# Kernel tuning notes

Measured on AMD Instinct MI355X. Metric: run time of the kernel, lower is better.

The kernel has to match this reference:

```python
import jax, jax.numpy as jnp
import numpy as np

B, LQ, LK, E, HID, H = 4, 1024, 2048, 512, 512, 8


def _ln(x, g, b, eps=1e-5):
    mu = jnp.mean(x, -1, keepdims=True)
    var = jnp.mean((x - mu) ** 2, -1, keepdims=True)
    return (x - mu) * jax.lax.rsqrt(var + eps) * g + b


def _mha(q_in, k_in, v_in, Wq, bq, Wk, bk, Wv, bv, Wo, bo, nheads, q_valid, k_valid):
    # torch nn.MultiheadAttention (batch_first, eval/dropout=0) math
    Bq, Lq, Em = q_in.shape
    Lk = k_in.shape[1]
    hd = Em // nheads
    q = (q_in @ Wq.T + bq).reshape(Bq, Lq, nheads, hd)
    k = (k_in @ Wk.T + bk).reshape(Bq, Lk, nheads, hd)
    v = (v_in @ Wv.T + bv).reshape(Bq, Lk, nheads, hd)
    scale = 1.0 / np.sqrt(hd).astype(np.float32)
    s = jnp.einsum('bqhd,bkhd->bhqk', q, k) * scale
    if k_valid is not None:
        # valid query rows may only attend to valid key columns
        s = jnp.where(k_valid[:, None, None, :], s, jnp.finfo(s.dtype).min)
    w = jax.nn.softmax(s, axis=-1)
    # rows beyond a sample's length are fully masked in the torch nested path
    # (softmax -> NaN, later nan_to_num'd to 0); we zero them directly.
    w = jnp.where(q_valid[:, None, :, None], w, 0.0)
    o = jnp.einsum('bhqk,bkhd->bqhd', w, v).reshape(Bq, Lq, Em)
    return o @ Wo.T + bo, jnp.mean(w, axis=1)  # weights averaged over heads


def setup_inputs() -> dict:
    key = jax.random.key(0)
    ks = jax.random.split(key, 32)
    p = lambda i, shape: 0.02 * jax.random.normal(ks[i], shape, dtype=jnp.float32)
    inp = {
        'queries': jax.random.normal(ks[0], (B, LQ, E), dtype=jnp.float32),
        'keys': jax.random.normal(ks[1], (B, LK, E), dtype=jnp.float32),
        'q_len': jax.random.randint(ks[2], (B,), 1, LQ + 1),
        # cross-attention params
        'cWq': p(3, (E, E)), 'cbq': jnp.zeros((E,)),
        'cWk': p(4, (E, E)), 'cbk': jnp.zeros((E,)),
        'cWv': p(5, (E, E)), 'cbv': jnp.zeros((E,)),
        'cWo': p(6, (E, E)), 'cbo': jnp.zeros((E,)),
        # self-attention params
        'sWq': p(7, (HID, HID)), 'sbq': jnp.zeros((HID,)),
        'sWk': p(8, (HID, HID)), 'sbk': jnp.zeros((HID,)),
        'sWv': p(9, (HID, HID)), 'sbv': jnp.zeros((HID,)),
        'sWo': p(10, (HID, HID)), 'sbo': jnp.zeros((HID,)),
        # ffn + norms
        'Wf': p(11, (HID, E)), 'bf': jnp.zeros((HID,)),
        'g_cross': jnp.ones((E,)), 'b_cross': jnp.zeros((E,)),
        'g_ffn': jnp.ones((HID,)), 'b_ffn': jnp.zeros((HID,)),
        'g_self': jnp.ones((HID,)), 'b_self': jnp.zeros((HID,)),
    }
    return inp


def reference(queries, keys, q_len,
              cWq, cbq, cWk, cbk, cWv, cbv, cWo, cbo,
              sWq, sbq, sWk, sbk, sWv, sbv, sWo, sbo,
              Wf, bf, g_cross, b_cross, g_ffn, b_ffn, g_self, b_self):
    valid = jnp.arange(LQ)[None, :] < q_len[:, None]  # [B, LQ] ragged lengths
    q = jnp.where(valid[..., None], queries, 0.0)     # nested -> padded with 0
    # cross attention: valid rows attend to ALL keys (per the nested mask)
    cross, weights = _mha(q, keys, keys, cWq, cbq, cWk, cbk, cWv, cbv, cWo, cbo,
                          H, valid, None)
    q = _ln(jax.nn.silu(cross + q), g_cross, b_cross)
    f = q @ Wf.T + bf
    q = _ln(jax.nn.silu(q + f), g_ffn, b_ffn)  # q_dim == hidden_dim branch
    q = jnp.where(valid[..., None], q, 0.0)    # torch.nan_to_num on padded rows
    # self attention: valid rows attend only to valid rows of the same sample
    so, _ = _mha(q, q, q, sWq, sbq, sWk, sbk, sWv, sbv, sWo, sbo, H, valid, valid)
    q = _ln(jax.nn.silu(q + so), g_self, b_self)
    q = jnp.where(valid[..., None], q, 0.0)    # padded rows discarded by unbind
    return q, weights
```

## Files before the change

kernel.cpp:

```cpp
#include <hip/hip_runtime.h>

#define BB 4
#define SLQ 1024
#define SLK 2048
#define EE 512
#define HH 8
#define HD 64

typedef unsigned short u16;
typedef __attribute__((ext_vector_type(8))) short s16x8;
typedef __attribute__((ext_vector_type(4))) float f32x4;

__device__ __forceinline__ float bf2f(u16 u) {
  union { unsigned int i; float f; } v; v.i = ((unsigned int)u) << 16; return v.f;
}
__device__ __forceinline__ u16 f2bf(float f) {
  union { float f; unsigned int i; } v; v.f = f;
  unsigned int i = v.i;
  return (u16)((i + 0x7fffu + ((i >> 16) & 1u)) >> 16);
}

__device__ __forceinline__ void async16(const u16* g, u16* l) {
  __builtin_amdgcn_global_load_lds(
      (const __attribute__((address_space(1))) unsigned int*)g,
      (__attribute__((address_space(3))) unsigned int*)l, 16, 0, 0);
}

template<int BM, int BN, int MODE, int SKIPQ>
__global__ __launch_bounds__(256, 2)
void gemm_nt(const u16* __restrict__ A, const u16* __restrict__ Bm,
             const float* __restrict__ bias, u16* __restrict__ C,
             int M, int N, int K, int lda, int ldb, int ldc,
             long sAz, long sBz, long sCz, float alpha, int Lsub,
             const int* __restrict__ qlen)
{
  constexpr int WTM = BM / 2, WTN = BN / 2;
  constexpr int MI = WTM / 16, NI = WTN / 16;

  const int z = blockIdx.z;
  const int tileM = blockIdx.y * BM;
  const int tileN = blockIdx.x * BN;

  if (SKIPQ == 1) { if (tileM >= qlen[z >> 3]) return; }
  if (SKIPQ == 2) { int b = tileM >> 10; if ((tileM & 1023) >= qlen[b]) return; }

  __shared__ __align__(16) u16 smem[(BM + BN) * 32];
  u16* ldsA = smem;
  u16* ldsB = smem + BM * 32;

  const int t = threadIdx.x;
  const int lane = t & 63;
  const int wave = t >> 6;
  const int waveM = wave >> 1;
  const int waveN = wave & 1;
  const int lm = lane & 15;
  const int kg = lane >> 4;

  const u16* Ab = A + (long)z * sAz + (long)tileM * lda;
  const u16* Bb = Bm + (long)z * sBz + (long)tileN * ldb;

  f32x4 acc[MI][NI];
#pragma unroll
  for (int i = 0; i < MI; ++i)
#pragma unroll
    for (int j = 0; j < NI; ++j) acc[i][j] = (f32x4){0.f, 0.f, 0.f, 0.f};

  for (int kt = 0; kt < K; kt += 32) {
    __syncthreads();
#pragma unroll
    for (int i = 0; i < (BM * 4) / 256; ++i) {
      int c = i * 256 + t;
      async16(Ab + (long)(c >> 2) * lda + kt + (c & 3) * 8, ldsA + (c - lane) * 8);
    }
#pragma unroll
    for (int i = 0; i < (BN * 4) / 256; ++i) {
      int c = i * 256 + t;
      async16(Bb + (long)(c >> 2) * ldb + kt + (c & 3) * 8, ldsB + (c - lane) * 8);
    }
    __syncthreads();

    s16x8 aF[MI], bF[NI];
#pragma unroll
    for (int i = 0; i < MI; ++i)
      aF[i] = *(const s16x8*)&ldsA[(waveM * WTM + i * 16 + lm) * 32 + kg * 8];
#pragma unroll
    for (int j = 0; j < NI; ++j)
      bF[j] = *(const s16x8*)&ldsB[(waveN * WTN + j * 16 + lm) * 32 + kg * 8];
#pragma unroll
    for (int i = 0; i < MI; ++i)
#pragma unroll
      for (int j = 0; j < NI; ++j)
        acc[i][j] = __builtin_amdgcn_mfma_f32_16x16x32_bf16(aF[i], bF[j], acc[i][j], 0, 0, 0);
  }

  if (MODE == 0) {
#pragma unroll
    for (int c = 0; c < BM / 32; ++c) {
      const int rlo = c * 32;
      __syncthreads();
#pragma unroll
      for (int i = 0; i < MI; ++i) {
        int mbase = waveM * WTM + i * 16;
        if (mbase >= rlo && mbase < rlo + 32) {
#pragma unroll
          for (int j = 0; j < NI; ++j) {
            int n = waveN * WTN + j * 16 + lm;
            float bv = bias ? bias[tileN + n] : 0.0f;
#pragma unroll
            for (int r = 0; r < 4; ++r) {
              int m = mbase + kg * 4 + r;
              smem[(m - rlo) * BN + n] = f2bf(acc[i][j][r] * alpha + bv);
            }
          }
        }
      }
      __syncthreads();
#pragma unroll
      for (int v = 0; v < (32 * BN) / (256 * 8); ++v) {
        int idx = v * 256 + t;
        int row = idx / (BN / 8), col8 = idx % (BN / 8);
        *(uint4*)&C[(long)z * sCz + (long)(tileM + rlo + row) * ldc + tileN + col8 * 8] =
            *(const uint4*)&smem[row * BN + col8 * 8];
      }
    }
  } else if (MODE == 2) {
    constexpr int PAD = BM + 8;
    const int bb = tileM / Lsub;
    const int l0 = tileM - bb * Lsub;
#pragma unroll
    for (int c = 0; c < BN / 32; ++c) {
      __syncthreads();
#pragma unroll
      for (int j = 0; j < NI; ++j) {
        int nloc = waveN * WTN + j * 16 + lm;
        if (nloc >= c * 32 && nloc < c * 32 + 32) {
          int nl = nloc - c * 32;
          float bv = bias ? bias[tileN + nloc] : 0.0f;
#pragma unroll
          for (int i = 0; i < MI; ++i)
#pragma unroll
            for (int r = 0; r < 4; ++r) {
              int mm = waveM * WTM + i * 16 + kg * 4 + r;
              smem[nl * PAD + mm] = f2bf(acc[i][j][r] * alpha + bv);
            }
        }
      }
      __syncthreads();
#pragma unroll
      for (int v = 0; v < (32 * BM) / (256 * 8); ++v) {
        int idx = v * 256 + t;
        int nl = idx / (BM / 8), m8 = idx % (BM / 8);
        int n = tileN + c * 32 + nl;
        int h = n >> 6, d = n & 63;
        *(uint4*)&C[((long)(bb * HH + h) * HD + d) * Lsub + l0 + m8 * 8] =
            *(const uint4*)&smem[nl * PAD + m8 * 8];
      }
    }
  } else {
#pragma unroll
    for (int j = 0; j < NI; ++j) {
      int n = tileN + waveN * WTN + j * 16 + lm;
      float bv = bias ? bias[n] : 0.0f;
#pragma unroll
      for (int i = 0; i < MI; ++i) {
#pragma unroll
        for (int r = 0; r < 4; ++r) {
          int m = tileM + waveM * WTM + i * 16 + kg * 4 + r;
          float v = acc[i][j][r] * alpha + bv;
          int b = m / Lsub, l = m - b * Lsub;
          int h = n >> 6, d = n & 63;
          C[(((long)(b * HH + h) * Lsub + l) << 6) + d] = f2bf(v);
        }
      }
    }
  }
}

__global__ __launch_bounds__(256)
void softmax_stats_wmean(const u16* __restrict__ S, float* __restrict__ outw,
                         float2* __restrict__ stats, const int* __restrict__ qlen) {
  int row = blockIdx.x;
  int b = row >> 10, q = row & 1023;
  int t = threadIdx.x, lane = t & 63, w = t >> 6;
  float* wr = outw + (long)row * SLK;
  if (q >= qlen[b]) {
    float4 z = {0.f, 0.f, 0.f, 0.f};
    *(float4*)(wr + t * 8) = z; *(float4*)(wr + t * 8 + 4) = z;
    return;
  }
  __shared__ float acc4[4][2048];
#pragma unroll
  for (int hh = 0; hh < 2; ++hh) {
    int h = 2 * w + hh;
    const u16* p = S + ((long)((b * HH + h) * SLQ + q)) * SLK;
    float x[4][8];
    float m = -1e30f;
#pragma unroll
    for (int c = 0; c < 4; ++c) {
      s16x8 v = *(const s16x8*)(p + c * 512 + lane * 8);
#pragma unroll
      for (int j = 0; j < 8; ++j) { x[c][j] = bf2f((u16)v[j]); m = fmaxf(m, x[c][j]); }
    }
#pragma unroll
    for (int o = 1; o <= 32; o <<= 1) m = fmaxf(m, __shfl_xor(m, o));
    float s = 0.f;
#pragma unroll
    for (int c = 0; c < 4; ++c)
#pragma unroll
      for (int j = 0; j < 8; ++j) { x[c][j] = __expf(x[c][j] - m); s += x[c][j]; }
#pragma unroll
    for (int o = 1; o <= 32; o <<= 1) s += __shfl_xor(s, o);
    if (lane == 0) stats[(long)(b * HH + h) * SLQ + q] = (float2){m, s};
    float sc = 0.125f / s;
#pragma unroll
    for (int c = 0; c < 4; ++c) {
      float4 v0 = {x[c][0] * sc, x[c][1] * sc, x[c][2] * sc, x[c][3] * sc};
      float4 v1 = {x[c][4] * sc, x[c][5] * sc, x[c][6] * sc, x[c][7] * sc};
      if (hh == 0) {
        *(float4*)&acc4[w][c * 512 + lane * 8] = v0;
        *(float4*)&acc4[w][c * 512 + lane * 8 + 4] = v1;
      } else {
        float4 a0 = *(const float4*)&acc4[w][c * 512 + lane * 8];
        float4 a1 = *(const float4*)&acc4[w][c * 512 + lane * 8 + 4];
        a0.x += v0.x; a0.y += v0.y; a0.z += v0.z; a0.w += v0.w;
        a1.x += v1.x; a1.y += v1.y; a1.z += v1.z; a1.w += v1.w;
        *(float4*)&acc4[w][c * 512 + lane * 8] = a0;
        *(float4*)&acc4[w][c * 512 + lane * 8 + 4] = a1;
      }
    }
  }
  __syncthreads();
#pragma unroll
  for (int u = 0; u < 2; ++u) {
    int k = t * 8 + u * 4;
    float4 s0 = *(const float4*)&acc4[0][k];
    float4 s1 = *(const float4*)&acc4[1][k];
    float4 s2 = *(const float4*)&acc4[2][k];
    float4 s3 = *(const float4*)&acc4[3][k];
    float4 o = {s0.x + s1.x + s2.x + s3.x, s0.y + s1.y + s2.y + s3.y,
                s0.z + s1.z + s2.z + s3.z, s0.w + s1.w + s2.w + s3.w};
    *(float4*)(wr + k) = o;
  }
}

__global__ __launch_bounds__(256, 2)
void pv_cross(const u16* __restrict__ S, const u16* __restrict__ Vt,
              const float2* __restrict__ stats, float* __restrict__ Opart,
              const int* __restrict__ qlen)
{
  const int qt = blockIdx.x;
  const int bh = blockIdx.y;
  const int kc = blockIdx.z;
  const int b = bh >> 3;
  if (qt * 64 >= qlen[b]) return;

  __shared__ __align__(16) u16 Vl[64 * 136];

  const int t = threadIdx.x, lane = t & 63, w = t >> 6;
  const int lm = lane & 15, quad = lane >> 4;

  const int qrow = qt * 64 + w * 16 + lm;
  const u16* Sb = S + ((long)bh * SLQ + qrow) * SLK;
  const u16* Vb = Vt + (long)bh * HD * SLK;
  const float mrow = stats[(long)bh * SLQ + qrow].x;

  f32x4 O[4];
#pragma unroll
  for (int n = 0; n < 4; ++n) O[n] = (f32x4){0.f, 0.f, 0.f, 0.f};

  for (int ks = 0; ks < 4; ++ks) {
    const int k0 = kc * 512 + ks * 128;
    __syncthreads();
    for (int c = t; c < 1024; c += 256) {
      int d = c >> 4, c16 = c & 15;
      *(uint4*)&Vl[d * 136 + c16 * 8] = *(const uint4*)(Vb + (long)d * SLK + k0 + c16 * 8);
    }
    __syncthreads();
#pragma unroll
    for (int kk = 0; kk < 4; ++kk) {
      s16x8 raw = *(const s16x8*)(Sb + k0 + kk * 32 + quad * 8);
      s16x8 aP;
#pragma unroll
      for (int j = 0; j < 8; ++j)
        aP[j] = (short)f2bf(__expf(bf2f((u16)raw[j]) - mrow));
#pragma unroll
      for (int n = 0; n < 4; ++n) {
        s16x8 bV = *(const s16x8*)&Vl[(n * 16 + lm) * 136 + kk * 32 + quad * 8];
        O[n] = __builtin_amdgcn_mfma_f32_16x16x32_bf16(aP, bV, O[n], 0, 0, 0);
      }
    }
  }

#pragma unroll
  for (int r = 0; r < 4; ++r) {
    int qr2 = qt * 64 + w * 16 + quad * 4 + r;
#pragma unroll
    for (int n = 0; n < 4; ++n)
      Opart[(((long)bh * SLQ + qr2) * 4 + kc) * 64 + n * 16 + lm] = O[n][r];
  }
}

__global__ __launch_bounds__(256)
void pv_combine_cross(const float* __restrict__ Opart, const float2* __restrict__ stats,
                      u16* __restrict__ attn, const int* __restrict__ qlen)
{
  int gr = blockIdx.x * 16 + (threadIdx.x >> 4);
  int bh = gr >> 10, q = gr & 1023;
  int b = bh >> 3, h = bh & 7;
  if (q >= qlen[b]) return;
  int d = (threadIdx.x & 15) * 4;
  float ax = 0.f, ay = 0.f, az = 0.f, aw = 0.f;
#pragma unroll
  for (int c = 0; c < 4; ++c) {
    float4 o = *(const float4*)&Opart[((long)gr * 4 + c) * 64 + d];
    ax += o.x; ay += o.y; az += o.z; aw += o.w;
  }
  float inv = 1.0f / stats[gr].y;
  unsigned int lo = (unsigned int)f2bf(ax * inv) | ((unsigned int)f2bf(ay * inv) << 16);
  unsigned int hi = (unsigned int)f2bf(az * inv) | ((unsigned int)f2bf(aw * inv) << 16);
  *(uint2*)&attn[((long)b * SLQ + q) * EE + h * HD + d] = (uint2){lo, hi};
}

__global__ __launch_bounds__(256, 3)
void self_flash_chunk(const u16* __restrict__ Qc, const u16* __restrict__ Kc,
                      const u16* __restrict__ Vt, float* __restrict__ Opart,
                      float* __restrict__ ml, const int* __restrict__ qlen)
{
  const int qt = blockIdx.x;
  const int bh = blockIdx.y;
  const int ck = blockIdx.z;
  const int b = bh >> 3;
  const int kmax = qlen[b];
  const int k0 = ck * 128;
  if (qt * 64 >= kmax || k0 >= kmax) return;

  __shared__ __align__(16) u16 Kt[128 * 72];
  __shared__ __align__(16) u16 Vl[64 * 136];
  __shared__ __align__(16) u16 Pl[4 * 16 * 136];

  const int t = threadIdx.x, lane = t & 63, w = t >> 6;
  const int col = lane & 15, quad = lane >> 4;

  const u16* Qb = Qc + (long)bh * SLQ * HD;
  const u16* Kb = Kc + (long)bh * SLQ * HD;
  const u16* Vb = Vt + (long)bh * HD * SLQ;

  for (int c = t; c < 1024; c += 256) {
    int r = c >> 3, c8 = c & 7;
    *(uint4*)&Kt[r * 72 + c8 * 8] = *(const uint4*)(Kb + (long)(k0 + r) * HD + c8 * 8);
  }
  for (int c = t; c < 1024; c += 256) {
    int d = c >> 4, c16 = c & 15;
    *(uint4*)&Vl[d * 136 + c16 * 8] = *(const uint4*)(Vb + (long)d * SLQ + k0 + c16 * 8);
  }
  s16x8 aQ[2];
#pragma unroll
  for (int kk = 0; kk < 2; ++kk)
    aQ[kk] = *(const s16x8*)(Qb + (long)(qt * 64 + w * 16 + col) * HD + kk * 32 + quad * 8);
  __syncthreads();

  f32x4 s[8];
#pragma unroll
  for (int j = 0; j < 8; ++j) s[j] = (f32x4){0.f, 0.f, 0.f, 0.f};
#pragma unroll
  for (int j = 0; j < 8; ++j)
#pragma unroll
    for (int kk = 0; kk < 2; ++kk) {
      s16x8 bK = *(const s16x8*)&Kt[(j * 16 + col) * 72 + kk * 32 + quad * 8];
      s[j] = __builtin_amdgcn_mfma_f32_16x16x32_bf16(aQ[kk], bK, s[j], 0, 0, 0);
    }
#pragma unroll
  for (int j = 0; j < 8; ++j) {
    bool ok = (k0 + j * 16 + col) < kmax;
#pragma unroll
    for (int r = 0; r < 4; ++r)
      s[j][r] = ok ? s[j][r] * 0.125f : -1e30f;
  }
  float mr[4], lr[4];
#pragma unroll
  for (int r = 0; r < 4; ++r) {
    float tm = s[0][r];
#pragma unroll
    for (int j = 1; j < 8; ++j) tm = fmaxf(tm, s[j][r]);
#pragma unroll
    for (int o = 1; o <= 8; o <<= 1) tm = fmaxf(tm, __shfl_xor(tm, o));
    mr[r] = tm;
    float ps = 0.f;
#pragma unroll
    for (int j = 0; j < 8; ++j) {
      float p = __expf(s[j][r] - tm);
      s[j][r] = p;
      ps += p;
    }
#pragma unroll
    for (int o = 1; o <= 8; o <<= 1) ps += __shfl_xor(ps, o);
    lr[r] = ps;
  }
  u16* Pw = Pl + w * 16 * 136;
#pragma unroll
  for (int j = 0; j < 8; ++j)
#pragma unroll
    for (int r = 0; r < 4; ++r)
      Pw[(quad * 4 + r) * 136 + j * 16 + col] = f2bf(s[j][r]);

  f32x4 O[4];
#pragma unroll
  for (int n = 0; n < 4; ++n) O[n] = (f32x4){0.f, 0.f, 0.f, 0.f};
#pragma unroll
  for (int kk = 0; kk < 4; ++kk) {
    s16x8 aP = *(const s16x8*)&Pw[col * 136 + kk * 32 + quad * 8];
#pragma unroll
    for (int n = 0; n < 4; ++n) {
      s16x8 bV = *(const s16x8*)&Vl[(n * 16 + col) * 136 + kk * 32 + quad * 8];
      O[n] = __builtin_amdgcn_mfma_f32_16x16x32_bf16(aP, bV, O[n], 0, 0, 0);
    }
  }
#pragma unroll
  for (int r = 0; r < 4; ++r) {
    int q = qt * 64 + w * 16 + quad * 4 + r;
    long gq = (long)bh * SLQ + q;
#pragma unroll
    for (int n = 0; n < 4; ++n)
      Opart[(gq * 8 + ck) * 64 + n * 16 + col] = O[n][r];
    if (col == 0) {
      ml[(gq * 8 + ck) * 2] = mr[r];
      ml[(gq * 8 + ck) * 2 + 1] = lr[r];
    }
  }
}

__global__ __launch_bounds__(256)
void self_combine(const float* __restrict__ Opart, const float* __restrict__ ml,
                  u16* __restrict__ attn, const int* __restrict__ qlen)
{
  int gr = blockIdx.x * 16 + (threadIdx.x >> 4);
  int bh = gr >> 10, q = gr & 1023;
  int b = bh >> 3, h = bh & 7;
  int kmax = qlen[b];
  if (q >= kmax) return;
  int NC = (kmax + 127) >> 7;
  int d = (threadIdx.x & 15) * 4;
  long base = (long)gr * 8;
  float M = -1e30f;
  for (int c = 0; c < NC; ++c) M = fmaxf(M, ml[(base + c) * 2]);
  float L = 0.f;
  float ax = 0.f, ay = 0.f, az = 0.f, aw = 0.f;
  for (int c = 0; c < NC; ++c) {
    float wgt = __expf(ml[(base + c) * 2] - M);
    L += ml[(base + c) * 2 + 1] * wgt;
    float4 o = *(const float4*)&Opart[(base + c) * 64 + d];
    ax += o.x * wgt; ay += o.y * wgt; az += o.z * wgt; aw += o.w * wgt;
  }
  float inv = 1.0f / L;
  unsigned int lo = (unsigned int)f2bf(ax * inv) | ((unsigned int)f2bf(ay * inv) << 16);
  unsigned int hi = (unsigned int)f2bf(az * inv) | ((unsigned int)f2bf(aw * inv) << 16);
  *(uint2*)&attn[((long)b * SLQ + q) * EE + h * HD + d] = (uint2){lo, hi};
}

__global__ __launch_bounds__(256)
void cvt_all(const float* __restrict__ queries, const float* __restrict__ keys,
             const int* __restrict__ qlen,
             const float* w0, const float* w1, const float* w2, const float* w3,
             const float* w4, const float* w5, const float* w6, const float* w7,
             const float* w8,
             u16* __restrict__ q0, u16* __restrict__ keysb, u16* __restrict__ Wb) {
  int blk = blockIdx.x;
  int t = threadIdx.x;
  const float* src;
  u16* dst;
  long off;
  bool mask = false;
  int b = 0, q = 0;
  if (blk < 1024) {
    off = (long)blk * 2048 + t * 8;
    int row = (int)(off >> 9);
    b = row >> 10; q = row & 1023;
    mask = true;
    src = queries; dst = q0;
  } else if (blk < 3072) {
    off = (long)(blk - 1024) * 2048 + t * 8;
    src = keys; dst = keysb;
  } else {
    int mat = (blk - 3072) >> 7, part = (blk - 3072) & 127;
    const float* srcs[9] = {w0, w1, w2, w3, w4, w5, w6, w7, w8};
    src = srcs[mat];
    off = (long)part * 2048 + t * 8;
    dst = Wb + (long)mat * EE * EE;
  }
  s16x8 o = (s16x8){0, 0, 0, 0, 0, 0, 0, 0};
  if (!mask || q < qlen[b]) {
    float4 a = *(const float4*)&src[off];
    float4 c = *(const float4*)&src[off + 4];
    o[0] = (short)f2bf(a.x); o[1] = (short)f2bf(a.y);
    o[2] = (short)f2bf(a.z); o[3] = (short)f2bf(a.w);
    o[4] = (short)f2bf(c.x); o[5] = (short)f2bf(c.y);
    o[6] = (short)f2bf(c.z); o[7] = (short)f2bf(c.w);
  }
  *(s16x8*)&dst[off] = o;
}

__device__ __forceinline__ float blockSum(float v, float* red4) {
#pragma unroll
  for (int o = 32; o; o >>= 1) v += __shfl_xor(v, o);
  if ((threadIdx.x & 63) == 0) red4[threadIdx.x >> 6] = v;
  __syncthreads();
  v = red4[0] + red4[1] + red4[2] + red4[3];
  __syncthreads();
  return v;
}

template<int OUTF32>
__global__ __launch_bounds__(256)
void silu_ln_kernel(const u16* __restrict__ x1, const u16* __restrict__ x2,
                    const float* __restrict__ g, const float* __restrict__ beta,
                    const int* __restrict__ qlen, void* __restrict__ outv, int mode) {
  int row = blockIdx.x;
  int b = row >> 10, q = row & 1023;
  int t = threadIdx.x;
  if (mode && q >= qlen[b]) {
    if (mode == 1) {
      if (OUTF32) {
        float* o = (float*)outv + (long)row * EE;
        o[2 * t] = 0.f; o[2 * t + 1] = 0.f;
      } else {
        u16* o = (u16*)outv + (long)row * EE;
        *(unsigned int*)&o[2 * t] = 0u;
      }
    }
    return;
  }
  __shared__ float red4[4];
  const u16* p1 = x1 + (long)row * EE;
  const u16* p2 = x2 + (long)row * EE;
  float a0 = bf2f(p1[2 * t]) + bf2f(p2[2 * t]);
  float a1 = bf2f(p1[2 * t + 1]) + bf2f(p2[2 * t + 1]);
  a0 = a0 / (1.f + __expf(-a0));
  a1 = a1 / (1.f + __expf(-a1));
  float mu = blockSum(a0 + a1, red4) * (1.f / 512.f);
  float d0 = a0 - mu, d1 = a1 - mu;
  float var = blockSum(d0 * d0 + d1 * d1, red4) * (1.f / 512.f);
  float rs = rsqrtf(var + 1e-5f);
  float r0 = d0 * rs * g[2 * t] + beta[2 * t];
  float r1 = d1 * rs * g[2 * t + 1] + beta[2 * t + 1];
  if (OUTF32) {
    float* o = (float*)outv + (long)row * EE;
    o[2 * t] = r0; o[2 * t + 1] = r1;
  } else {
    u16* o = (u16*)outv + (long)row * EE;
    o[2 * t] = f2bf(r0); o[2 * t + 1] = f2bf(r1);
  }
}

extern "C" void kernel_launch(void* const* d_in, const int* in_sizes, int n_in,
                              void* d_out, int out_size, void* d_ws, size_t ws_size,
                              hipStream_t stream) {
  const float* queries = (const float*)d_in[0];
  const float* keys    = (const float*)d_in[1];
  const int*   qlen    = (const int*)d_in[2];
  const float* cWq = (const float*)d_in[3],  *cbq = (const float*)d_in[4];
  const float* cWk = (const float*)d_in[5],  *cbk = (const float*)d_in[6];
  const float* cWv = (const float*)d_in[7],  *cbv = (const float*)d_in[8];
  const float* cWo = (const float*)d_in[9],  *cbo = (const float*)d_in[10];
  const float* sWq = (const float*)d_in[11], *sbq = (const float*)d_in[12];
  const float* sWk = (const float*)d_in[13], *sbk = (const float*)d_in[14];
  const float* sWv = (const float*)d_in[15], *sbv = (const float*)d_in[16];
  const float* sWo = (const float*)d_in[17], *sbo = (const float*)d_in[18];
  const float* Wf  = (const float*)d_in[19], *bfb = (const float*)d_in[20];
  const float* g_cross = (const float*)d_in[21], *b_cross = (const float*)d_in[22];
  const float* g_ffn   = (const float*)d_in[23], *b_ffn   = (const float*)d_in[24];
  const float* g_self  = (const float*)d_in[25], *b_self  = (const float*)d_in[26];

  float* out_q = (float*)d_out;
  float* out_w = out_q + (long)BB * SLQ * EE;

  u16* ws = (u16*)d_ws;
  u16* S     = ws;
  u16* Qc    = S   + (long)BB * HH * SLQ * SLK;
  u16* Kc    = Qc  + (long)BB * HH * SLQ * HD;
  u16* Vt    = Kc  + (long)BB * HH * SLK * HD;
  u16* q0    = Vt  + (long)BB * HH * SLK * HD;
  u16* keysb = q0  + (long)BB * SLQ * EE;
  u16* attn  = keysb + (long)BB * SLK * EE;
  u16* proj  = attn + (long)BB * SLQ * EE;
  u16* q1    = proj + (long)BB * SLQ * EE;
  u16* fbuf  = q1  + (long)BB * SLQ * EE;
  u16* q2    = fbuf + (long)BB * SLQ * EE;
  u16* Wb    = q2  + (long)BB * SLQ * EE;
  const long WSLOT = (long)EE * EE;
  float*  CpF  = (float*)(Wb + 9 * WSLOT);
  float2* stat = (float2*)(CpF + 8388608);

  float* OpS = (float*)S;
  float* mlS = (float*)(S + 33554432);

  u16* bWq = Wb + 0 * WSLOT; u16* bWk = Wb + 1 * WSLOT; u16* bWv = Wb + 2 * WSLOT;
  u16* bWo = Wb + 3 * WSLOT; u16* bsWq = Wb + 4 * WSLOT; u16* bsWk = Wb + 5 * WSLOT;
  u16* bsWv = Wb + 6 * WSLOT; u16* bsWo = Wb + 7 * WSLOT; u16* bWf = Wb + 8 * WSLOT;

  dim3 blk(256);
  const int MQ = BB * SLQ;
  const int MK = BB * SLK;

  cvt_all<<<dim3(3072 + 9 * 128), blk, 0, stream>>>(
      queries, keys, qlen, cWq, cWk, cWv, cWo, sWq, sWk, sWv, sWo, Wf, q0, keysb, Wb);

  gemm_nt<64, 64, 1, 2><<<dim3(EE / 64, MQ / 64, 1), blk, 0, stream>>>(
      q0, bWq, cbq, Qc, MQ, EE, EE, EE, EE, 0, 0, 0, 0, 1.0f, SLQ, qlen);
  gemm_nt<64, 64, 1, 0><<<dim3(EE / 64, MK / 64, 1), blk, 0, stream>>>(
      keysb, bWk, cbk, Kc, MK, EE, EE, EE, EE, 0, 0, 0, 0, 1.0f, SLK, qlen);
  gemm_nt<64, 64, 2, 0><<<dim3(EE / 64, MK / 64, 1), blk, 0, stream>>>(
      keysb, bWv, cbv, Vt, MK, EE, EE, EE, EE, 0, 0, 0, 0, 1.0f, SLK, qlen);

  gemm_nt<128, 128, 0, 1><<<dim3(SLK / 128, SLQ / 128, BB * HH), blk, 0, stream>>>(
      Qc, Kc, nullptr, S, SLQ, SLK, HD, HD, HD, SLK,
      (long)SLQ * HD, (long)SLK * HD, (long)SLQ * SLK, 0.125f, 0, qlen);

  softmax_stats_wmean<<<dim3(BB * SLQ), blk, 0, stream>>>(S, out_w, stat, qlen);

  pv_cross<<<dim3(16, 32, 4), blk, 0, stream>>>(S, Vt, stat, CpF, qlen);
  pv_combine_cross<<<dim3(2048), blk, 0, stream>>>(CpF, stat, attn, qlen);

  gemm_nt<64, 64, 0, 2><<<dim3(EE / 64, MQ / 64, 1), blk, 0, stream>>>(
      attn, bWo, cbo, proj, MQ, EE, EE, EE, EE, EE, 0, 0, 0, 1.0f, SLQ, qlen);

  silu_ln_kernel<0><<<dim3(MQ), blk, 0, stream>>>(proj, q0, g_cross, b_cross, qlen, q1, 2);

  gemm_nt<64, 64, 0, 2><<<dim3(EE / 64, MQ / 64, 1), blk, 0, stream>>>(
      q1, bWf, bfb, fbuf, MQ, EE, EE, EE, EE, EE, 0, 0, 0, 1.0f, SLQ, qlen);

  silu_ln_kernel<0><<<dim3(MQ), blk, 0, stream>>>(q1, fbuf, g_ffn, b_ffn, qlen, q2, 1);

  gemm_nt<64, 64, 1, 2><<<dim3(EE / 64, MQ / 64, 1), blk, 0, stream>>>(
      q2, bsWq, sbq, Qc, MQ, EE, EE, EE, EE, 0, 0, 0, 0, 1.0f, SLQ, qlen);
  gemm_nt<64, 64, 1, 2><<<dim3(EE / 64, MQ / 64, 1), blk, 0, stream>>>(
      q2, bsWk, sbk, Kc, MQ, EE, EE, EE, EE, 0, 0, 0, 0, 1.0f, SLQ, qlen);
  gemm_nt<64, 64, 2, 2><<<dim3(EE / 64, MQ / 64, 1), blk, 0, stream>>>(
      q2, bsWv, sbv, Vt, MQ, EE, EE, EE, EE, 0, 0, 0, 0, 1.0f, SLQ, qlen);

  self_flash_chunk<<<dim3(16, 32, 8), blk, 0, stream>>>(Qc, Kc, Vt, OpS, mlS, qlen);
  self_combine<<<dim3(2048), blk, 0, stream>>>(OpS, mlS, attn, qlen);

  gemm_nt<64, 64, 0, 2><<<dim3(EE / 64, MQ / 64, 1), blk, 0, stream>>>(
      attn, bsWo, sbo, proj, MQ, EE, EE, EE, EE, EE, 0, 0, 0, 1.0f, SLQ, qlen);

  silu_ln_kernel<1><<<dim3(MQ), blk, 0, stream>>>(q2, proj, g_self, b_self, qlen, out_q, 1);
}
```

Before: 349.5 us.

## Batch QKV projections, bf16 partials, per-wave epilogue, longer self-attn chunks

```diff
diff --git a/kernel.cpp b/kernel.cpp
--- a/kernel.cpp
+++ b/kernel.cpp
@@ -36,6 +36,10 @@
 {
   constexpr int WTM = BM / 2, WTN = BN / 2;
   constexpr int MI = WTM / 16, NI = WTN / 16;
+  constexpr int EPAD = WTN + 8;
+  constexpr int SM1 = (BM + BN) * 32;
+  constexpr int SM2 = (MODE == 0) ? 4 * WTM * EPAD : 0;
+  constexpr int SM = (SM1 > SM2) ? SM1 : SM2;
 
   const int z = blockIdx.z;
   const int tileM = blockIdx.y * BM;
@@ -44,7 +48,7 @@
   if (SKIPQ == 1) { if (tileM >= qlen[z >> 3]) return; }
   if (SKIPQ == 2) { int b = tileM >> 10; if ((tileM & 1023) >= qlen[b]) return; }
 
-  __shared__ __align__(16) u16 smem[(BM + BN) * 32];
+  __shared__ __align__(16) u16 smem[SM];
   u16* ldsA = smem;
   u16* ldsB = smem + BM * 32;
 
@@ -94,36 +98,132 @@
   }
 
   if (MODE == 0) {
-#pragma unroll
-    for (int c = 0; c < BM / 32; ++c) {
-      const int rlo = c * 32;
-      __syncthreads();
+    u16* ep = smem + wave * (WTM * EPAD);
+    __syncthreads();
+#pragma unroll
+    for (int i = 0; i < MI; ++i)
+#pragma unroll
+      for (int j = 0; j < NI; ++j) {
+        int n = waveN * WTN + j * 16 + lm;
+        float bv = bias ? bias[tileN + n] : 0.0f;
+#pragma unroll
+        for (int r = 0; r < 4; ++r)
+          ep[(i * 16 + kg * 4 + r) * EPAD + j * 16 + lm] = f2bf(acc[i][j][r] * alpha + bv);
+      }
+    const long Crow = (long)z * sCz + (long)(tileM + waveM * WTM) * ldc + tileN + waveN * WTN;
+#pragma unroll
+    for (int it = 0; it < (WTM * WTN) / 512; ++it) {
+      int idx = it * 64 + lane;
+      int row = idx / (WTN / 8), seg = idx % (WTN / 8);
+      *(uint4*)&C[Crow + (long)row * ldc + seg * 8] =
+          *(const uint4*)&ep[row * EPAD + seg * 8];
+    }
+  } else {
+#pragma unroll
+    for (int j = 0; j < NI; ++j) {
+      int n = tileN + waveN * WTN + j * 16 + lm;
+      float bv = bias ? bias[n] : 0.0f;
 #pragma unroll
       for (int i = 0; i < MI; ++i) {
-        int mbase = waveM * WTM + i * 16;
-        if (mbase >= rlo && mbase < rlo + 32) {
-#pragma unroll
-          for (int j = 0; j < NI; ++j) {
-            int n = waveN * WTN + j * 16 + lm;
-            float bv = bias ? bias[tileN + n] : 0.0f;
-#pragma unroll
-            for (int r = 0; r < 4; ++r) {
-              int m = mbase + kg * 4 + r;
-              smem[(m - rlo) * BN + n] = f2bf(acc[i][j][r] * alpha + bv);
-            }
-          }
+#pragma unroll
+        for (int r = 0; r < 4; ++r) {
+          int m = tileM + waveM * WTM + i * 16 + kg * 4 + r;
+          float v = acc[i][j][r] * alpha + bv;
+          int b = m / Lsub, l = m - b * Lsub;
+          int h = n >> 6, d = n & 63;
+          C[(((long)(b * HH + h) * Lsub + l) << 6) + d] = f2bf(v);
         }
       }
-      __syncthreads();
-#pragma unroll
-      for (int v = 0; v < (32 * BN) / (256 * 8); ++v) {
-        int idx = v * 256 + t;
-        int row = idx / (BN / 8), col8 = idx % (BN / 8);
-        *(uint4*)&C[(long)z * sCz + (long)(tileM + rlo + row) * ldc + tileN + col8 * 8] =
-            *(const uint4*)&smem[row * BN + col8 * 8];
-      }
-    }
-  } else if (MODE == 2) {
+    }
+  }
+}
+
+template<int BM, int BN, int SKIPQ, int NPROJ>
+__global__ __launch_bounds__(256, 2)
+void gemm_proj(const u16* __restrict__ A,
+               const u16* B0, const u16* B1, const u16* B2,
+               const float* bias0, const float* bias1, const float* bias2,
+               u16* C0, u16* C1, u16* C2,
+               int M, int lda, int Lsub, const int* __restrict__ qlen)
+{
+  constexpr int WTM = BM / 2, WTN = BN / 2;
+  constexpr int MI = WTM / 16, NI = WTN / 16;
+
+  const int z = blockIdx.z;
+  const int tileM = blockIdx.y * BM;
+  const int tileN = blockIdx.x * BN;
+  if (SKIPQ == 2) { int b = tileM >> 10; if ((tileM & 1023) >= qlen[b]) return; }
+
+  const u16* Bm = (z == 0) ? B0 : (z == 1) ? B1 : B2;
+  const float* bias = (z == 0) ? bias0 : (z == 1) ? bias1 : bias2;
+  u16* C = (z == 0) ? C0 : (z == 1) ? C1 : C2;
+  const bool tr = (z == NPROJ - 1);
+
+  __shared__ __align__(16) u16 smem[(BM + BN) * 32];
+  u16* ldsA = smem;
+  u16* ldsB = smem + BM * 32;
+
+  const int t = threadIdx.x;
+  const int lane = t & 63;
+  const int wave = t >> 6;
+  const int waveM = wave >> 1;
+  const int waveN = wave & 1;
+  const int lm = lane & 15;
+  const int kg = lane >> 4;
+
+  const u16* Ab = A + (long)tileM * lda;
+  const u16* Bb = Bm + (long)tileN * EE;
+
+  f32x4 acc[MI][NI];
+#pragma unroll
+  for (int i = 0; i < MI; ++i)
+#pragma unroll
+    for (int j = 0; j < NI; ++j) acc[i][j] = (f32x4){0.f, 0.f, 0.f, 0.f};
+
+  for (int kt = 0; kt < EE; kt += 32) {
+    __syncthreads();
+#pragma unroll
+    for (int i = 0; i < (BM * 4) / 256; ++i) {
+      int c = i * 256 + t;
+      async16(Ab + (long)(c >> 2) * lda + kt + (c & 3) * 8, ldsA + (c - lane) * 8);
+    }
+#pragma unroll
+    for (int i = 0; i < (BN * 4) / 256; ++i) {
+      int c = i * 256 + t;
+      async16(Bb + (long)(c >> 2) * EE + kt + (c & 3) * 8, ldsB + (c - lane) * 8);
+    }
+    __syncthreads();
+
+    s16x8 aF[MI], bF[NI];
+#pragma unroll
+    for (int i = 0; i < MI; ++i)
+      aF[i] = *(const s16x8*)&ldsA[(waveM * WTM + i * 16 + lm) * 32 + kg * 8];
+#pragma unroll
+    for (int j = 0; j < NI; ++j)
+      bF[j] = *(const s16x8*)&ldsB[(waveN * WTN + j * 16 + lm) * 32 + kg * 8];
+#pragma unroll
+    for (int i = 0; i < MI; ++i)
+#pragma unroll
+      for (int j = 0; j < NI; ++j)
+        acc[i][j] = __builtin_amdgcn_mfma_f32_16x16x32_bf16(aF[i], bF[j], acc[i][j], 0, 0, 0);
+  }
+
+  if (!tr) {
+#pragma unroll
+    for (int j = 0; j < NI; ++j) {
+      int n = tileN + waveN * WTN + j * 16 + lm;
+      float bv = bias[n];
+#pragma unroll
+      for (int i = 0; i < MI; ++i)
+#pragma unroll
+        for (int r = 0; r < 4; ++r) {
+          int m = tileM + waveM * WTM + i * 16 + kg * 4 + r;
+          int b = m / Lsub, l = m - b * Lsub;
+          int h = n >> 6, d = n & 63;
+          C[(((long)(b * HH + h) * Lsub + l) << 6) + d] = f2bf(acc[i][j][r] + bv);
+        }
+    }
+  } else {
     constexpr int PAD = BM + 8;
     const int bb = tileM / Lsub;
     const int l0 = tileM - bb * Lsub;
@@ -135,13 +235,13 @@
         int nloc = waveN * WTN + j * 16 + lm;
         if (nloc >= c * 32 && nloc < c * 32 + 32) {
           int nl = nloc - c * 32;
-          float bv = bias ? bias[tileN + nloc] : 0.0f;
+          float bv = bias[tileN + nloc];
 #pragma unroll
           for (int i = 0; i < MI; ++i)
 #pragma unroll
             for (int r = 0; r < 4; ++r) {
               int mm = waveM * WTM + i * 16 + kg * 4 + r;
-              smem[nl * PAD + mm] = f2bf(acc[i][j][r] * alpha + bv);
+              smem[nl * PAD + mm] = f2bf(acc[i][j][r] + bv);
             }
         }
       }
@@ -154,23 +254,6 @@
         int h = n >> 6, d = n & 63;
         *(uint4*)&C[((long)(bb * HH + h) * HD + d) * Lsub + l0 + m8 * 8] =
             *(const uint4*)&smem[nl * PAD + m8 * 8];
-      }
-    }
-  } else {
-#pragma unroll
-    for (int j = 0; j < NI; ++j) {
-      int n = tileN + waveN * WTN + j * 16 + lm;
-      float bv = bias ? bias[n] : 0.0f;
-#pragma unroll
-      for (int i = 0; i < MI; ++i) {
-#pragma unroll
-        for (int r = 0; r < 4; ++r) {
-          int m = tileM + waveM * WTM + i * 16 + kg * 4 + r;
-          float v = acc[i][j][r] * alpha + bv;
-          int b = m / Lsub, l = m - b * Lsub;
-          int h = n >> 6, d = n & 63;
-          C[(((long)(b * HH + h) * Lsub + l) << 6) + d] = f2bf(v);
-        }
       }
     }
   }
@@ -245,7 +328,7 @@
 
 __global__ __launch_bounds__(256, 2)
 void pv_cross(const u16* __restrict__ S, const u16* __restrict__ Vt,
-              const float2* __restrict__ stats, float* __restrict__ Opart,
+              const float2* __restrict__ stats, u16* __restrict__ Opart,
               const int* __restrict__ qlen)
 {
   const int qt = blockIdx.x;
@@ -296,12 +379,12 @@
     int qr2 = qt * 64 + w * 16 + quad * 4 + r;
 #pragma unroll
     for (int n = 0; n < 4; ++n)
-      Opart[(((long)bh * SLQ + qr2) * 4 + kc) * 64 + n * 16 + lm] = O[n][r];
+      Opart[(((long)bh * SLQ + qr2) * 4 + kc) * 64 + n * 16 + lm] = f2bf(O[n][r]);
   }
 }
 
 __global__ __launch_bounds__(256)
-void pv_combine_cross(const float* __restrict__ Opart, const float2* __restrict__ stats,
+void pv_combine_cross(const u16* __restrict__ Opart, const float2* __restrict__ stats,
                       u16* __restrict__ attn, const int* __restrict__ qlen)
 {
   int gr = blockIdx.x * 16 + (threadIdx.x >> 4);
@@ -312,8 +395,8 @@
   float ax = 0.f, ay = 0.f, az = 0.f, aw = 0.f;
 #pragma unroll
   for (int c = 0; c < 4; ++c) {
-    float4 o = *(const float4*)&Opart[((long)gr * 4 + c) * 64 + d];
-    ax += o.x; ay += o.y; az += o.z; aw += o.w;
+    const u16* p = Opart + ((long)gr * 4 + c) * 64 + d;
+    ax += bf2f(p[0]); ay += bf2f(p[1]); az += bf2f(p[2]); aw += bf2f(p[3]);
   }
   float inv = 1.0f / stats[gr].y;
   unsigned int lo = (unsigned int)f2bf(ax * inv) | ((unsigned int)f2bf(ay * inv) << 16);
@@ -323,16 +406,15 @@
 
 __global__ __launch_bounds__(256, 3)
 void self_flash_chunk(const u16* __restrict__ Qc, const u16* __restrict__ Kc,
-                      const u16* __restrict__ Vt, float* __restrict__ Opart,
-                      float* __restrict__ ml, const int* __restrict__ qlen)
+                      const u16* __restrict__ Vt, u16* __restrict__ Opart,
+                      float2* __restrict__ ml, const int* __restrict__ qlen)
 {
   const int qt = blockIdx.x;
   const int bh = blockIdx.y;
   const int ck = blockIdx.z;
   const int b = bh >> 3;
   const int kmax = qlen[b];
-  const int k0 = ck * 128;
-  if (qt * 64 >= kmax || k0 >= kmax) return;
+  if (qt * 64 >= kmax || ck * 256 >= kmax) return;
 
   __shared__ __align__(16) u16 Kt[128 * 72];
   __shared__ __align__(16) u16 Vl[64 * 136];
@@ -345,92 +427,103 @@
   const u16* Kb = Kc + (long)bh * SLQ * HD;
   const u16* Vb = Vt + (long)bh * HD * SLQ;
 
-  for (int c = t; c < 1024; c += 256) {
-    int r = c >> 3, c8 = c & 7;
-    *(uint4*)&Kt[r * 72 + c8 * 8] = *(const uint4*)(Kb + (long)(k0 + r) * HD + c8 * 8);
-  }
-  for (int c = t; c < 1024; c += 256) {
-    int d = c >> 4, c16 = c & 15;
-    *(uint4*)&Vl[d * 136 + c16 * 8] = *(const uint4*)(Vb + (long)d * SLQ + k0 + c16 * 8);
-  }
   s16x8 aQ[2];
 #pragma unroll
   for (int kk = 0; kk < 2; ++kk)
     aQ[kk] = *(const s16x8*)(Qb + (long)(qt * 64 + w * 16 + col) * HD + kk * 32 + quad * 8);
-  __syncthreads();
-
-  f32x4 s[8];
-#pragma unroll
-  for (int j = 0; j < 8; ++j) s[j] = (f32x4){0.f, 0.f, 0.f, 0.f};
-#pragma unroll
-  for (int j = 0; j < 8; ++j)
-#pragma unroll
-    for (int kk = 0; kk < 2; ++kk) {
-      s16x8 bK = *(const s16x8*)&Kt[(j * 16 + col) * 72 + kk * 32 + quad * 8];
-      s[j] = __builtin_amdgcn_mfma_f32_16x16x32_bf16(aQ[kk], bK, s[j], 0, 0, 0);
-    }
-#pragma unroll
-  for (int j = 0; j < 8; ++j) {
-    bool ok = (k0 + j * 16 + col) < kmax;
-#pragma unroll
-    for (int r = 0; r < 4; ++r)
-      s[j][r] = ok ? s[j][r] * 0.125f : -1e30f;
-  }
+
+  f32x4 O[4];
   float mr[4], lr[4];
 #pragma unroll
-  for (int r = 0; r < 4; ++r) {
-    float tm = s[0][r];
-#pragma unroll
-    for (int j = 1; j < 8; ++j) tm = fmaxf(tm, s[j][r]);
-#pragma unroll
-    for (int o = 1; o <= 8; o <<= 1) tm = fmaxf(tm, __shfl_xor(tm, o));
-    mr[r] = tm;
-    float ps = 0.f;
+  for (int n = 0; n < 4; ++n) O[n] = (f32x4){0.f, 0.f, 0.f, 0.f};
+#pragma unroll
+  for (int r = 0; r < 4; ++r) { mr[r] = -1e30f; lr[r] = 0.f; }
+
+  u16* Pw = Pl + w * 16 * 136;
+
+  for (int kt = 0; kt < 2; ++kt) {
+    const int k0 = ck * 256 + kt * 128;
+    if (k0 >= kmax) break;
+    __syncthreads();
+    for (int c = t; c < 1024; c += 256) {
+      int r = c >> 3, c8 = c & 7;
+      *(uint4*)&Kt[r * 72 + c8 * 8] = *(const uint4*)(Kb + (long)(k0 + r) * HD + c8 * 8);
+    }
+    for (int c = t; c < 1024; c += 256) {
+      int d = c >> 4, c16 = c & 15;
+      *(uint4*)&Vl[d * 136 + c16 * 8] = *(const uint4*)(Vb + (long)d * SLQ + k0 + c16 * 8);
+    }
+    __syncthreads();
+
+    f32x4 s[8];
+#pragma unroll
+    for (int j = 0; j < 8; ++j) s[j] = (f32x4){0.f, 0.f, 0.f, 0.f};
+#pragma unroll
+    for (int j = 0; j < 8; ++j)
+#pragma unroll
+      for (int kk = 0; kk < 2; ++kk) {
+        s16x8 bK = *(const s16x8*)&Kt[(j * 16 + col) * 72 + kk * 32 + quad * 8];
+        s[j] = __builtin_amdgcn_mfma_f32_16x16x32_bf16(aQ[kk], bK, s[j], 0, 0, 0);
+      }
 #pragma unroll
     for (int j = 0; j < 8; ++j) {
-      float p = __expf(s[j][r] - tm);
-      s[j][r] = p;
-      ps += p;
-    }
-#pragma unroll
-    for (int o = 1; o <= 8; o <<= 1) ps += __shfl_xor(ps, o);
-    lr[r] = ps;
-  }
-  u16* Pw = Pl + w * 16 * 136;
-#pragma unroll
-  for (int j = 0; j < 8; ++j)
-#pragma unroll
-    for (int r = 0; r < 4; ++r)
-      Pw[(quad * 4 + r) * 136 + j * 16 + col] = f2bf(s[j][r]);
-
-  f32x4 O[4];
-#pragma unroll
-  for (int n = 0; n < 4; ++n) O[n] = (f32x4){0.f, 0.f, 0.f, 0.f};
-#pragma unroll
-  for (int kk = 0; kk < 4; ++kk) {
-    s16x8 aP = *(const s16x8*)&Pw[col * 136 + kk * 32 + quad * 8];
-#pragma unroll
-    for (int n = 0; n < 4; ++n) {
-      s16x8 bV = *(const s16x8*)&Vl[(n * 16 + col) * 136 + kk * 32 + quad * 8];
-      O[n] = __builtin_amdgcn_mfma_f32_16x16x32_bf16(aP, bV, O[n], 0, 0, 0);
-    }
-  }
+      bool ok = (k0 + j * 16 + col) < kmax;
+#pragma unroll
+      for (int r = 0; r < 4; ++r)
+        s[j][r] = ok ? s[j][r] * 0.125f : -1e30f;
+    }
+#pragma unroll
+    for (int r = 0; r < 4; ++r) {
+      float tm = s[0][r];
+#pragma unroll
+      for (int j = 1; j < 8; ++j) tm = fmaxf(tm, s[j][r]);
+#pragma unroll
+      for (int o = 1; o <= 8; o <<= 1) tm = fmaxf(tm, __shfl_xor(tm, o));
+      float mnew = fmaxf(mr[r], tm);
+      float alpha = __expf(mr[r] - mnew);
+      mr[r] = mnew;
+      float ps = 0.f;
+#pragma unroll
+      for (int j = 0; j < 8; ++j) {
+        float p = __expf(s[j][r] - mnew);
+        s[j][r] = p;
+        ps += p;
+      }
+#pragma unroll
+      for (int o = 1; o <= 8; o <<= 1) ps += __shfl_xor(ps, o);
+      lr[r] = lr[r] * alpha + ps;
+#pragma unroll
+      for (int n = 0; n < 4; ++n) O[n][r] *= alpha;
+    }
+#pragma unroll
+    for (int j = 0; j < 8; ++j)
+#pragma unroll
+      for (int r = 0; r < 4; ++r)
+        Pw[(quad * 4 + r) * 136 + j * 16 + col] = f2bf(s[j][r]);
+#pragma unroll
+    for (int kk = 0; kk < 4; ++kk) {
+      s16x8 aP = *(const s16x8*)&Pw[col * 136 + kk * 32 + quad * 8];
+#pragma unroll
+      for (int n = 0; n < 4; ++n) {
+        s16x8 bV = *(const s16x8*)&Vl[(n * 16 + col) * 136 + kk * 32 + quad * 8];
+        O[n] = __builtin_amdgcn_mfma_f32_16x16x32_bf16(aP, bV, O[n], 0, 0, 0);
+      }
+    }
+  }
+
 #pragma unroll
   for (int r = 0; r < 4; ++r) {
     int q = qt * 64 + w * 16 + quad * 4 + r;
     long gq = (long)bh * SLQ + q;
 #pragma unroll
     for (int n = 0; n < 4; ++n)
-      Opart[(gq * 8 + ck) * 64 + n * 16 + col] = O[n][r];
-    if (col == 0) {
-      ml[(gq * 8 + ck) * 2] = mr[r];
-      ml[(gq * 8 + ck) * 2 + 1] = lr[r];
-    }
+      Opart[(gq * 4 + ck) * 64 + n * 16 + col] = f2bf(O[n][r]);
+    if (col == 0) ml[gq * 4 + ck] = (float2){mr[r], lr[r]};
   }
 }
 
 __global__ __launch_bounds__(256)
-void self_combine(const float* __restrict__ Opart, const float* __restrict__ ml,
+void self_combine(const u16* __restrict__ Opart, const float2* __restrict__ ml,
                   u16* __restrict__ attn, const int* __restrict__ qlen)
 {
   int gr = blockIdx.x * 16 + (threadIdx.x >> 4);
@@ -438,18 +531,20 @@
   int b = bh >> 3, h = bh & 7;
   int kmax = qlen[b];
   if (q >= kmax) return;
-  int NC = (kmax + 127) >> 7;
+  int NC = (kmax + 255) >> 8;
   int d = (threadIdx.x & 15) * 4;
-  long base = (long)gr * 8;
+  long base = (long)gr * 4;
   float M = -1e30f;
-  for (int c = 0; c < NC; ++c) M = fmaxf(M, ml[(base + c) * 2]);
+  for (int c = 0; c < NC; ++c) M = fmaxf(M, ml[base + c].x);
   float L = 0.f;
   float ax = 0.f, ay = 0.f, az = 0.f, aw = 0.f;
   for (int c = 0; c < NC; ++c) {
-    float wgt = __expf(ml[(base + c) * 2] - M);
-    L += ml[(base + c) * 2 + 1] * wgt;
-    float4 o = *(const float4*)&Opart[(base + c) * 64 + d];
-    ax += o.x * wgt; ay += o.y * wgt; az += o.z * wgt; aw += o.w * wgt;
+    float2 st = ml[base + c];
+    float wgt = __expf(st.x - M);
+    L += st.y * wgt;
+    const u16* p = Opart + (base + c) * 64 + d;
+    ax += bf2f(p[0]) * wgt; ay += bf2f(p[1]) * wgt;
+    az += bf2f(p[2]) * wgt; aw += bf2f(p[3]) * wgt;
   }
   float inv = 1.0f / L;
   unsigned int lo = (unsigned int)f2bf(ax * inv) | ((unsigned int)f2bf(ay * inv) << 16);
@@ -587,11 +682,11 @@
   u16* q2    = fbuf + (long)BB * SLQ * EE;
   u16* Wb    = q2  + (long)BB * SLQ * EE;
   const long WSLOT = (long)EE * EE;
-  float*  CpF  = (float*)(Wb + 9 * WSLOT);
-  float2* stat = (float2*)(CpF + 8388608);
-
-  float* OpS = (float*)S;
-  float* mlS = (float*)(S + 33554432);
+  u16*    Cpb  = Wb + 9 * WSLOT;
+  float2* stat = (float2*)(Cpb + 8388608);
+
+  u16*    OpS = S;
+  float2* mlS = (float2*)(S + 8388608);
 
   u16* bWq = Wb + 0 * WSLOT; u16* bWk = Wb + 1 * WSLOT; u16* bWv = Wb + 2 * WSLOT;
   u16* bWo = Wb + 3 * WSLOT; u16* bsWq = Wb + 4 * WSLOT; u16* bsWk = Wb + 5 * WSLOT;
@@ -606,10 +701,8 @@
 
   gemm_nt<64, 64, 1, 2><<<dim3(EE / 64, MQ / 64, 1), blk, 0, stream>>>(
       q0, bWq, cbq, Qc, MQ, EE, EE, EE, EE, 0, 0, 0, 0, 1.0f, SLQ, qlen);
-  gemm_nt<64, 64, 1, 0><<<dim3(EE / 64, MK / 64, 1), blk, 0, stream>>>(
-      keysb, bWk, cbk, Kc, MK, EE, EE, EE, EE, 0, 0, 0, 0, 1.0f, SLK, qlen);
-  gemm_nt<64, 64, 2, 0><<<dim3(EE / 64, MK / 64, 1), blk, 0, stream>>>(
-      keysb, bWv, cbv, Vt, MK, EE, EE, EE, EE, 0, 0, 0, 0, 1.0f, SLK, qlen);
+  gemm_proj<64, 64, 0, 2><<<dim3(EE / 64, MK / 64, 2), blk, 0, stream>>>(
+      keysb, bWk, bWv, nullptr, cbk, cbv, nullptr, Kc, Vt, nullptr, MK, EE, SLK, qlen);
 
   gemm_nt<128, 128, 0, 1><<<dim3(SLK / 128, SLQ / 128, BB * HH), blk, 0, stream>>>(
       Qc, Kc, nullptr, S, SLQ, SLK, HD, HD, HD, SLK,
@@ -617,8 +710,8 @@
 
   softmax_stats_wmean<<<dim3(BB * SLQ), blk, 0, stream>>>(S, out_w, stat, qlen);
 
-  pv_cross<<<dim3(16, 32, 4), blk, 0, stream>>>(S, Vt, stat, CpF, qlen);
-  pv_combine_cross<<<dim3(2048), blk, 0, stream>>>(CpF, stat, attn, qlen);
+  pv_cross<<<dim3(16, 32, 4), blk, 0, stream>>>(S, Vt, stat, Cpb, qlen);
+  pv_combine_cross<<<dim3(2048), blk, 0, stream>>>(Cpb, stat, attn, qlen);
 
   gemm_nt<64, 64, 0, 2><<<dim3(EE / 64, MQ / 64, 1), blk, 0, stream>>>(
       attn, bWo, cbo, proj, MQ, EE, EE, EE, EE, EE, 0, 0, 0, 1.0f, SLQ, qlen);
@@ -630,14 +723,10 @@
 
   silu_ln_kernel<0><<<dim3(MQ), blk, 0, stream>>>(q1, fbuf, g_ffn, b_ffn, qlen, q2, 1);
 
-  gemm_nt<64, 64, 1, 2><<<dim3(EE / 64, MQ / 64, 1), blk, 0, stream>>>(
-      q2, bsWq, sbq, Qc, MQ, EE, EE, EE, EE, 0, 0, 0, 0, 1.0f, SLQ, qlen);
-  gemm_nt<64, 64, 1, 2><<<dim3(EE / 64, MQ / 64, 1), blk, 0, stream>>>(
-      q2, bsWk, sbk, Kc, MQ, EE, EE, EE, EE, 0, 0, 0, 0, 1.0f, SLQ, qlen);
-  gemm_nt<64, 64, 2, 2><<<dim3(EE / 64, MQ / 64, 1), blk, 0, stream>>>(
-      q2, bsWv, sbv, Vt, MQ, EE, EE, EE, EE, 0, 0, 0, 0, 1.0f, SLQ, qlen);
-
-  self_flash_chunk<<<dim3(16, 32, 8), blk, 0, stream>>>(Qc, Kc, Vt, OpS, mlS, qlen);
+  gemm_proj<64, 64, 2, 3><<<dim3(EE / 64, MQ / 64, 3), blk, 0, stream>>>(
+      q2, bsWq, bsWk, bsWv, sbq, sbk, sbv, Qc, Kc, Vt, MQ, EE, SLQ, qlen);
+
+  self_flash_chunk<<<dim3(16, 32, 4), blk, 0, stream>>>(Qc, Kc, Vt, OpS, mlS, qlen);
   self_combine<<<dim3(2048), blk, 0, stream>>>(OpS, mlS, attn, qlen);
 
   gemm_nt<64, 64, 0, 2><<<dim3(EE / 64, MQ / 64, 1), blk, 0, stream>>>(
```

Result: faster. 320.4 us (-8.3%).
